# Performance work log

Measured on AMD Instinct MI355X. Metric: run time of the kernel, lower is better.

The kernel has to match this reference:

```python
import jax, jax.numpy as jnp
import numpy as np

B, S, D = 2, 2048, 4096
N_HEADS, N_KV_HEADS = 32, 8
HEAD_DIM = D // N_HEADS  # 128
N_REP = N_HEADS // N_KV_HEADS
NEG_INF = -1e9  # finite stand-in for -inf additive causal mask


def apply_rotary_emb(x, freqs_cis):
    # x: [b, s, h, hd]; freqs_cis: [s, hd//2, 2] (cos, sin)
    b, s, h, hd = x.shape
    xr = x.reshape(b, s, h, hd // 2, 2)
    fc = freqs_cis.reshape(1, s, 1, hd // 2, 2)
    o0 = xr[..., 0] * fc[..., 0] - xr[..., 1] * fc[..., 1]
    o1 = xr[..., 1] * fc[..., 0] + xr[..., 0] * fc[..., 1]
    return jnp.stack([o0, o1], axis=-1).reshape(b, s, h, hd)


def setup_inputs() -> dict:
    key = jax.random.key(0)
    ks = jax.random.split(key, 6)
    x = jax.random.normal(ks[0], (B, S, D), dtype=jnp.float32)
    # weights stored torch-style: [out_features, in_features]
    wq = jax.random.normal(ks[1], (N_HEADS * HEAD_DIM, D), dtype=jnp.float32) * 0.02
    wk = jax.random.normal(ks[2], (N_KV_HEADS * HEAD_DIM, D), dtype=jnp.float32) * 0.02
    wv = jax.random.normal(ks[3], (N_KV_HEADS * HEAD_DIM, D), dtype=jnp.float32) * 0.02
    wo = jax.random.normal(ks[4], (D, N_HEADS * HEAD_DIM), dtype=jnp.float32) * 0.02
    # rotary table (Llama-style, theta=10000)
    inv_freq = 1.0 / (10000.0 ** (np.arange(0, HEAD_DIM, 2, dtype=np.float32) / HEAD_DIM))
    angles = np.arange(S, dtype=np.float32)[:, None] * inv_freq[None, :]
    freqs_cis = jnp.asarray(np.stack([np.cos(angles), np.sin(angles)], axis=-1))  # [S, hd//2, 2]
    # additive causal mask
    mask = jnp.where(jnp.tril(jnp.ones((S, S), dtype=bool)), 0.0, NEG_INF).astype(jnp.float32)
    return {"x": x, "start_pos": 0, "freqs_cis": freqs_cis, "mask": mask,
            "wq": wq, "wk": wk, "wv": wv, "wo": wo}


def reference(x, start_pos, freqs_cis, mask, wq, wk, wv, wo):
    b, s, _ = x.shape
    xq = jnp.einsum('bsd,ed->bse', x, wq).reshape(b, s, N_HEADS, HEAD_DIM)
    xk = jnp.einsum('bsd,ed->bse', x, wk).reshape(b, s, N_KV_HEADS, HEAD_DIM)
    xv = jnp.einsum('bsd,ed->bse', x, wv).reshape(b, s, N_KV_HEADS, HEAD_DIM)
    xq = apply_rotary_emb(xq, freqs_cis)
    xk = apply_rotary_emb(xk, freqs_cis)
    # repeat_kv (repeat_interleave along head dim)
    xk = jnp.repeat(xk, N_REP, axis=2)
    xv = jnp.repeat(xv, N_REP, axis=2)
    q = xq.transpose(0, 2, 1, 3)  # [b, h, s, hd]
    k = xk.transpose(0, 2, 1, 3)
    v = xv.transpose(0, 2, 1, 3)
    scores = jnp.einsum('bhqd,bhkd->bhqk', q, k) / jnp.sqrt(jnp.float32(HEAD_DIM))
    scores = scores + mask[None, None, :, :]
    probs = jax.nn.softmax(scores.astype(jnp.float32), axis=-1).astype(q.dtype)
    out = jnp.einsum('bhqk,bhkd->bhqd', probs, v)
    out = out.transpose(0, 2, 1, 3).reshape(b, s, N_HEADS * HEAD_DIM)
    return jnp.einsum('bse,de->bsd', out, wo)
```

## Files before the change

kernel.cpp:

```cpp
#include <hip/hip_runtime.h>
#include <cstdint>
#include <cstddef>

#define B_   2
#define S_   2048
#define D_   4096
#define H_   32
#define KVH_ 8
#define HD_  128

typedef unsigned short u16;
typedef short     bf16x8 __attribute__((ext_vector_type(8)));
typedef float     f32x4  __attribute__((ext_vector_type(4)));
typedef float     f32x16 __attribute__((ext_vector_type(16)));
typedef u16       u16x8  __attribute__((ext_vector_type(8)));
typedef uint32_t  u32x2  __attribute__((ext_vector_type(2)));
typedef uint32_t  u32x4  __attribute__((ext_vector_type(4)));

__device__ __forceinline__ u16 f2bf(float f) {
  union { float f; uint32_t u; } v; v.f = f;
  uint32_t u = v.u;
  return (u16)((u + 0x7fffu + ((u >> 16) & 1u)) >> 16);
}
__device__ __forceinline__ float bf2f(u16 h) {
  union { uint32_t u; float f; } v; v.u = ((uint32_t)h) << 16;
  return v.f;
}
__device__ __forceinline__ uint32_t cvtpk(float lo, float hi_) {
  uint32_t r; asm("v_cvt_pk_bf16_f32 %0, %1, %2" : "=v"(r) : "v"(lo), "v"(hi_)); return r;
}
__device__ __forceinline__ float exp2v(float x) {
  float r; asm("v_exp_f32 %0, %1" : "=v"(r) : "v"(x)); return r;
}

__device__ __forceinline__ void gl_lds16(const void* g, void* l) {
  __builtin_amdgcn_global_load_lds(
      (const __attribute__((address_space(1))) void*)g,
      (__attribute__((address_space(3))) void*)l, 16, 0, 0);
}

#define MFMA(a, b, c)  __builtin_amdgcn_mfma_f32_16x16x32_bf16((a), (b), (c), 0, 0, 0)
#define MFMA32(a, b, c) __builtin_amdgcn_mfma_f32_32x32x16_bf16((a), (b), (c), 0, 0, 0)
#define PLSWAP(x, y) asm volatile("v_permlane32_swap_b32 %0, %1" : "+v"(x), "+v"(y))

__global__ void cast4_kernel(const float* __restrict__ x, const float* __restrict__ wq,
                             const float* __restrict__ wk, const float* __restrict__ wv,
                             u16* __restrict__ xb, u16* __restrict__ wqb,
                             u16* __restrict__ wkb, u16* __restrict__ wvb) {
  int i = blockIdx.x * 256 + threadIdx.x;
  const float* src; u16* dst; int off;
  if (i < 2097152)      { src = x;  dst = xb;  off = i; }
  else if (i < 4194304) { src = wq; dst = wqb; off = i - 2097152; }
  else if (i < 4718592) { src = wk; dst = wkb; off = i - 4194304; }
  else                  { src = wv; dst = wvb; off = i - 4718592; }
  const float4* p = (const float4*)src + (size_t)off * 2;
  float4 a = p[0], b = p[1];
  u16x8 r;
  r[0] = f2bf(a.x); r[1] = f2bf(a.y); r[2] = f2bf(a.z); r[3] = f2bf(a.w);
  r[4] = f2bf(b.x); r[5] = f2bf(b.y); r[6] = f2bf(b.z); r[7] = f2bf(b.w);
  *((u16x8*)dst + off) = r;
}

__global__ void cast_kernel(const float* __restrict__ in, u16* __restrict__ out, int n8) {
  int i = blockIdx.x * blockDim.x + threadIdx.x;
  if (i >= n8) return;
  const float4* p = (const float4*)in + (size_t)i * 2;
  float4 a = p[0], b = p[1];
  u16x8 r;
  r[0] = f2bf(a.x); r[1] = f2bf(a.y); r[2] = f2bf(a.z); r[3] = f2bf(a.w);
  r[4] = f2bf(b.x); r[5] = f2bf(b.y); r[6] = f2bf(b.z); r[7] = f2bf(b.w);
  *((u16x8*)out + i) = r;
}

template <bool OUT_F32>
__global__ __launch_bounds__(256, 2)
void gemm_bt(const u16* __restrict__ A, const u16* __restrict__ Bw,
             void* __restrict__ C, int M, int N, int K) {
  __shared__ u16 lA[128 * 32];
  __shared__ u16 lB[128 * 32];
  const int tid = threadIdx.x;
  const int w = tid >> 6, l = tid & 63;
  const int lc = l & 15, lg = l >> 4;
  const int bn = blockIdx.x, bm = blockIdx.y;
  const int wr = w >> 1, wc = w & 1;
  const u16* Ab = A + (size_t)(bm * 128) * K;
  const u16* Bb = Bw + (size_t)(bn * 128) * K;
  const int srow = l >> 2;
  const int scol = (l & 3) * 8;

  f32x4 acc[4][4];
#pragma unroll
  for (int i = 0; i < 4; ++i)
#pragma unroll
    for (int j = 0; j < 4; ++j) acc[i][j] = (f32x4){0.f, 0.f, 0.f, 0.f};

  const int nk = K >> 5;
  for (int kt = 0; kt < nk; ++kt) {
    const int k0 = kt * 32;
    __syncthreads();
#pragma unroll
    for (int i = 0; i < 2; ++i) {
      const int rowA = (w * 2 + i) * 16;
      gl_lds16(Ab + (size_t)(rowA + srow) * K + k0 + scol, &lA[rowA * 32]);
      gl_lds16(Bb + (size_t)(rowA + srow) * K + k0 + scol, &lB[rowA * 32]);
    }
    __syncthreads();
    bf16x8 af[4], bfr[4];
#pragma unroll
    for (int mi = 0; mi < 4; ++mi)
      af[mi] = *(const bf16x8*)&lA[(wr * 64 + mi * 16 + lc) * 32 + lg * 8];
#pragma unroll
    for (int ni = 0; ni < 4; ++ni)
      bfr[ni] = *(const bf16x8*)&lB[(wc * 64 + ni * 16 + lc) * 32 + lg * 8];
#pragma unroll
    for (int mi = 0; mi < 4; ++mi)
#pragma unroll
      for (int ni = 0; ni < 4; ++ni)
        acc[mi][ni] = MFMA(af[mi], bfr[ni], acc[mi][ni]);
  }

#pragma unroll
  for (int mi = 0; mi < 4; ++mi)
#pragma unroll
    for (int ni = 0; ni < 4; ++ni)
#pragma unroll
      for (int r = 0; r < 4; ++r) {
        const int row = bm * 128 + wr * 64 + mi * 16 + lg * 4 + r;
        const int col = bn * 128 + wc * 64 + ni * 16 + lc;
        if constexpr (OUT_F32)
          ((float*)C)[(size_t)row * N + col] = acc[mi][ni][r];
        else
          ((u16*)C)[(size_t)row * N + col] = f2bf(acc[mi][ni][r]);
      }
}

template <int MODE>
__global__ __launch_bounds__(512, 2)
void gemm256_bt(const u16* __restrict__ A, const u16* __restrict__ Bw,
                void* __restrict__ C, int M, int N, int K,
                const float* __restrict__ fr, float qscale) {
  __shared__ u16 sA[2 * 256 * 64];
  __shared__ u16 sB[2 * 256 * 64];
  const int tid = threadIdx.x;
  const int w = tid >> 6, l = tid & 63;
  const int lc = l & 15, lg = l >> 4;
  const int wm = w >> 2, wn = w & 3;
  const int nbn = N >> 8;
  const int nwg = (M >> 8) * nbn;
  const int cpx = nwg >> 3;
  const int lin = blockIdx.x;
  const int swz = (lin & 7) * cpx + (lin >> 3);
  const int bm = swz / nbn, bn = swz % nbn;
  const u16* Ab = A + (size_t)(bm * 256) * K;
  const u16* Bb = Bw + (size_t)(bn * 256) * K;
  const int lr = l >> 3;
  const int scc = ((l & 7) ^ lr) * 8;
  int cxg[2];
#pragma unroll
  for (int kk = 0; kk < 2; ++kk) cxg[kk] = ((kk * 4 + lg) ^ (lc & 7)) * 8;

  f32x4 acc[8][4];
#pragma unroll
  for (int i = 0; i < 8; ++i)
#pragma unroll
    for (int j = 0; j < 4; ++j) acc[i][j] = (f32x4){0.f, 0.f, 0.f, 0.f};

  auto STAGEA = [&](int buf, int t1, int h) {
    const int k0 = t1 * 64;
#pragma unroll
    for (int j = 0; j < 2; ++j) {
      const int r0 = h * 128 + w * 16 + j * 8;
      gl_lds16(Ab + (size_t)(r0 + lr) * K + k0 + scc, &sA[buf * 16384 + r0 * 64]);
    }
  };
  auto STAGEB = [&](int buf, int t1, int h) {
    const int k0 = t1 * 64;
#pragma unroll
    for (int j = 0; j < 2; ++j) {
      const int r0 = h * 128 + w * 16 + j * 8;
      gl_lds16(Bb + (size_t)(r0 + lr) * K + k0 + scc, &sB[buf * 16384 + r0 * 64]);
    }
  };

  bf16x8 a0r[4][2], a1r[4][2], b0r[2][2], b1r[2][2];
  auto LDA0 = [&](int cb) {
#pragma unroll
    for (int mi = 0; mi < 4; ++mi)
#pragma unroll
      for (int kk = 0; kk < 2; ++kk)
        a0r[mi][kk] = *(const bf16x8*)
            &sA[cb + (wm * 64 + mi * 16 + lc) * 64 + cxg[kk]];
  };
  auto LDA1 = [&](int cb) {
#pragma unroll
    for (int mi = 0; mi < 4; ++mi)
#pragma unroll
      for (int kk = 0; kk < 2; ++kk)
        a1r[mi][kk] = *(const bf16x8*)
            &sA[cb + (128 + wm * 64 + mi * 16 + lc) * 64 + cxg[kk]];
  };
  auto LDB0 = [&](int cb) {
#pragma unroll
    for (int ni = 0; ni < 2; ++ni)
#pragma unroll
      for (int kk = 0; kk < 2; ++kk)
        b0r[ni][kk] = *(const bf16x8*)
            &sB[cb + (wn * 32 + ni * 16 + lc) * 64 + cxg[kk]];
  };
  auto LDB1 = [&](int cb) {
#pragma unroll
    for (int ni = 0; ni < 2; ++ni)
#pragma unroll
      for (int kk = 0; kk < 2; ++kk)
        b1r[ni][kk] = *(const bf16x8*)
            &sB[cb + (128 + wn * 32 + ni * 16 + lc) * 64 + cxg[kk]];
  };

#define VMW(N_) asm volatile("s_waitcnt vmcnt(" #N_ ")" ::: "memory")
#define BARR do { __builtin_amdgcn_s_barrier(); asm volatile("" ::: "memory"); } while (0)
#define LGKM do { asm volatile("s_waitcnt lgkmcnt(0)" ::: "memory"); \
                  __builtin_amdgcn_sched_barrier(0); } while (0)
#define MMQ(AF, HA, HB, BF) do { __builtin_amdgcn_s_setprio(1); \
  _Pragma("unroll") for (int kk = 0; kk < 2; ++kk) \
  _Pragma("unroll") for (int mi = 0; mi < 4; ++mi) \
  _Pragma("unroll") for (int ni = 0; ni < 2; ++ni) \
    acc[(HA) * 4 + mi][(HB) * 2 + ni] = \
        MFMA(AF[mi][kk], BF[ni][kk], acc[(HA) * 4 + mi][(HB) * 2 + ni]); \
  __builtin_amdgcn_s_setprio(0); } while (0)

  const int nk = K >> 6;
  STAGEA(0, 0, 0); STAGEB(0, 0, 0);
  STAGEB(0, 0, 1); STAGEA(0, 0, 1);
  STAGEA(1, 1, 0); STAGEB(1, 1, 0);
  VMW(4);
  BARR;

  for (int t = 0; t < nk; ++t) {
    const int cur = t & 1;
    const int cb = cur * 16384;
    const int nb = cur ^ 1;
    const bool n1 = (t + 1 < nk), n2 = (t + 2 < nk);

    LDA0(cb); LDB0(cb);
    BARR;
    if (n1) { STAGEB(nb, t + 1, 1); STAGEA(nb, t + 1, 1); }
    LGKM;
    MMQ(a0r, 0, 0, b0r);

    LDB1(cb);
    BARR;
    LGKM;
    MMQ(a0r, 0, 1, b1r);

    LDA1(cb);
    BARR;
    if (n2) STAGEA(cur, t + 2, 0);
    LGKM;
    MMQ(a1r, 1, 1, b1r);

    if (n2) STAGEB(cur, t + 2, 0);
    MMQ(a1r, 1, 0, b0r);
    if (n1) {
      if (n2) VMW(4); else VMW(0);
      BARR;
    }
  }
#undef VMW
#undef BARR
#undef LGKM
#undef MMQ

#pragma unroll
  for (int ha = 0; ha < 2; ++ha)
#pragma unroll
    for (int mi = 0; mi < 4; ++mi)
#pragma unroll
      for (int hb = 0; hb < 2; ++hb)
#pragma unroll
        for (int ni = 0; ni < 2; ++ni)
#pragma unroll
          for (int r = 0; r < 4; ++r) {
            const int row = bm * 256 + ha * 128 + wm * 64 + mi * 16 + lg * 4 + r;
            const int col = bn * 256 + hb * 128 + wn * 32 + ni * 16 + lc;
            const float v = acc[ha * 4 + mi][hb * 2 + ni][r];
            if constexpr (MODE == 1) {
              ((float*)C)[(size_t)row * N + col] = v;
            } else if constexpr (MODE == 0) {
              ((u16*)C)[(size_t)row * N + col] = f2bf(v);
            } else {
              const float pv = __shfl_xor(v, 1, 64);
              const int b = row >> 11, s = row & (S_ - 1);
              const int h = col >> 7, d = col & 127;
              const float2 cs = ((const float2*)fr)[s * 64 + (d >> 1)];
              const float o = ((lc & 1) == 0) ? (v * cs.x - pv * cs.y)
                                              : (v * cs.x + pv * cs.y);
              ((u16*)C)[(((size_t)(b * H_ + h) * S_ + s)) * HD_ + d] =
                  f2bf(o * qscale);
            }
          }
}

template <int NH, int STRIDE, int OFF>
__global__ void rope_kernel(const u16* __restrict__ lin, const float* __restrict__ fr,
                            u16* __restrict__ out, float scale) {
  int idx = blockIdx.x * 256 + threadIdx.x;
  const int total = B_ * S_ * NH * 64;
  if (idx >= total) return;
  const int i = idx & 63;
  const int h = (idx >> 6) % NH;
  const int t = idx / (64 * NH);
  const int s = t & (S_ - 1);
  const int b = t >> 11;
  const size_t src = (size_t)t * STRIDE + OFF + h * HD_ + 2 * i;
  const float x0 = bf2f(lin[src]);
  const float x1 = bf2f(lin[src + 1]);
  const float2 cs = ((const float2*)fr)[s * 64 + i];
  const float o0 = (x0 * cs.x - x1 * cs.y) * scale;
  const float o1 = (x1 * cs.x + x0 * cs.y) * scale;
  const size_t dst = ((size_t)((b * NH + h) * S_ + s)) * HD_ + 2 * i;
  out[dst] = f2bf(o0);
  out[dst + 1] = f2bf(o1);
}

__global__ void vtrans_kernel(const u16* __restrict__ kvlin, u16* __restrict__ vt) {
  __shared__ u16 tile[32][33];
  const int tx = threadIdx.x, ty = threadIdx.y;
  const int s0 = blockIdx.x * 32;
  const int d0 = blockIdx.y * 32;
  const int bk = blockIdx.z;
  const int b = bk >> 3, kv = bk & 7;
#pragma unroll
  for (int r = 0; r < 4; ++r) {
    const int s = s0 + ty + r * 8;
    tile[ty + r * 8][tx] =
        kvlin[((size_t)(b * S_ + s)) * 2048 + 1024 + kv * HD_ + d0 + tx];
  }
  __syncthreads();
#pragma unroll
  for (int r = 0; r < 4; ++r) {
    const int d = d0 + ty + r * 8;
    vt[((size_t)bk * HD_ + d) * S_ + s0 + tx] = tile[tx][ty + r * 8];
  }
}

__global__ __launch_bounds__(256, 2)
void attn_kernel(const u16* __restrict__ Q, const u16* __restrict__ K,
                 const u16* __restrict__ V, u16* __restrict__ O) {
  __shared__ u16 sK[2][64 * HD_];
  __shared__ u16 sV[2][HD_ * 64];
  const int tid = threadIdx.x;
  const int w = tid >> 6, l = tid & 63;
  const int hi = l >> 5, q32 = l & 31;
  const int kv = blockIdx.y, b = blockIdx.z;
  const int h = kv * 4 + w;
  const u16* Kp = K + ((size_t)(b * KVH_ + kv) * S_) * HD_;
  const u16* Vp = V + ((size_t)(b * KVH_ + kv) * HD_) * S_;

  int koff[4], voff[4];
#pragma unroll
  for (int i = 0; i < 4; ++i) {
    const int kr = w * 16 + i * 4 + (l >> 4);
    koff[i] = kr * HD_ + (((l & 15) ^ (kr & 7))) * 8;
    const int vr = w * 32 + i * 8 + (l >> 3);
    voff[i] = vr * S_ + (((l & 7) ^ (vr & 7))) * 8;
  }
  int cx[8];
#pragma unroll
  for (int c = 0; c < 8; ++c) cx[c] = ((c * 2 + hi) ^ (l & 7)) * 8;

  auto STAGE = [&](int bufi, int ti) {
    const u16* kg = Kp + (size_t)ti * (64 * HD_);
    const u16* vg = Vp + (size_t)ti * 64;
#pragma unroll
    for (int i = 0; i < 4; ++i) {
      gl_lds16(kg + koff[i], &sK[bufi][(w * 16 + i * 4) * HD_]);
      gl_lds16(vg + voff[i], &sV[bufi][(w * 32 + i * 8) * 64]);
    }
  };

  int cur = 0;
  for (int seg = 0; seg < 2; ++seg) {
    const int qt = seg ? (63 - blockIdx.x) : blockIdx.x;
    const int qg = qt * 32 + q32;
    const u16* Qp = Q + ((size_t)(b * H_ + h) * S_ + qt * 32) * HD_;

    bf16x8 qf[8];
#pragma unroll
    for (int ds = 0; ds < 8; ++ds)
      qf[ds] = *(const bf16x8*)(Qp + (size_t)q32 * HD_ + ds * 16 + hi * 8);
    asm volatile("s_waitcnt vmcnt(0)" ::: "memory");

    f32x16 out[4];
#pragma unroll
    for (int d = 0; d < 4; ++d)
#pragma unroll
      for (int r = 0; r < 16; ++r) out[d][r] = 0.f;
    float mrun = -1e30f, lrun = 0.f;

    const int nt = (qt >> 1) + 1;
    STAGE(cur, 0);

    for (int t = 0; t < nt; ++t) {
      if (t + 1 < nt) {
        STAGE(cur ^ 1, t + 1);
        asm volatile("s_waitcnt vmcnt(8)" ::: "memory");
      } else {
        asm volatile("s_waitcnt vmcnt(0)" ::: "memory");
      }
      __builtin_amdgcn_s_barrier();
      asm volatile("" ::: "memory");

      f32x16 sc0, sc1;
#pragma unroll
      for (int r = 0; r < 16; ++r) { sc0[r] = 0.f; sc1[r] = 0.f; }
      __builtin_amdgcn_s_setprio(1);
#pragma unroll
      for (int ds = 0; ds < 8; ++ds) {
        bf16x8 kf0 = *(const bf16x8*)&sK[cur][q32 * HD_ + cx[ds]];
        bf16x8 kf1 = *(const bf16x8*)&sK[cur][(32 + q32) * HD_ + cx[ds]];
        sc0 = MFMA32(kf0, qf[ds], sc0);
        sc1 = MFMA32(kf1, qf[ds], sc1);
      }
      __builtin_amdgcn_s_setprio(0);

      const bool diag = (t == nt - 1);
      float p0[16], p1[16];
#pragma unroll
      for (int r = 0; r < 16; ++r) {
        const int krow = (r & 3) + 8 * (r >> 2) + 4 * hi;
        float v0 = sc0[r], v1 = sc1[r];
        if (diag) {
          if (t * 64 + krow > qg) v0 = -1e9f;
          if (t * 64 + 32 + krow > qg) v1 = -1e9f;
        }
        p0[r] = v0; p1[r] = v1;
      }
      float rm = -1e30f;
#pragma unroll
      for (int r = 0; r < 16; ++r) rm = fmaxf(rm, fmaxf(p0[r], p1[r]));
      rm = fmaxf(rm, __shfl_xor(rm, 32, 64));
      if (!__all(rm <= mrun + 8.0f)) {
        const float mnew = fmaxf(mrun, rm);
        const float alpha = exp2v(mrun - mnew);
        mrun = mnew;
        lrun *= alpha;
#pragma unroll
        for (int d = 0; d < 4; ++d) out[d] *= alpha;
      }
      float sum = 0.f;
#pragma unroll
      for (int r = 0; r < 16; ++r) {
        p0[r] = exp2v(p0[r] - mrun);
        p1[r] = exp2v(p1[r] - mrun);
        sum += p0[r] + p1[r];
      }
      sum += __shfl_xor(sum, 32, 64);
      lrun += sum;
      uint32_t pk0[8], pk1[8];
#pragma unroll
      for (int g = 0; g < 4; ++g) {
        pk0[2 * g]     = cvtpk(p0[4 * g], p0[4 * g + 1]);
        pk0[2 * g + 1] = cvtpk(p0[4 * g + 2], p0[4 * g + 3]);
        pk1[2 * g]     = cvtpk(p1[4 * g], p1[4 * g + 1]);
        pk1[2 * g + 1] = cvtpk(p1[4 * g + 2], p1[4 * g + 3]);
      }
      PLSWAP(pk0[0], pk0[2]); PLSWAP(pk0[1], pk0[3]);
      PLSWAP(pk0[4], pk0[6]); PLSWAP(pk0[5], pk0[7]);
      PLSWAP(pk1[0], pk1[2]); PLSWAP(pk1[1], pk1[3]);
      PLSWAP(pk1[4], pk1[6]); PLSWAP(pk1[5], pk1[7]);
      bf16x8 pa[4];
      pa[0] = __builtin_bit_cast(bf16x8, (u32x4){pk0[0], pk0[1], pk0[2], pk0[3]});
      pa[1] = __builtin_bit_cast(bf16x8, (u32x4){pk0[4], pk0[5], pk0[6], pk0[7]});
      pa[2] = __builtin_bit_cast(bf16x8, (u32x4){pk1[0], pk1[1], pk1[2], pk1[3]});
      pa[3] = __builtin_bit_cast(bf16x8, (u32x4){pk1[4], pk1[5], pk1[6], pk1[7]});
      __builtin_amdgcn_s_setprio(1);
#pragma unroll
      for (int d = 0; d < 4; ++d) {
        const int vbase = (d * 32 + q32) * 64;
#pragma unroll
        for (int kk = 0; kk < 4; ++kk) {
          bf16x8 vf = *(const bf16x8*)&sV[cur][vbase + cx[kk]];
          out[d] = MFMA32(vf, pa[kk], out[d]);
        }
      }
      __builtin_amdgcn_s_setprio(0);
      asm volatile("" ::: "memory");
      __builtin_amdgcn_s_barrier();
      cur ^= 1;
    }

    const float inv = 1.0f / lrun;
    u16* myS = ((u16*)sK) + w * 4096;
#pragma unroll
    for (int d = 0; d < 4; ++d)
#pragma unroll
      for (int rq = 0; rq < 4; ++rq) {
        u32x2 pw;
        pw[0] = cvtpk(out[d][rq * 4 + 0] * inv, out[d][rq * 4 + 1] * inv);
        pw[1] = cvtpk(out[d][rq * 4 + 2] * inv, out[d][rq * 4 + 3] * inv);
        const int gin = (d * 8 + rq * 2 + hi) ^ (q32 & 15);
        *(u32x2*)&myS[q32 * 128 + gin * 4] = pw;
      }
    asm volatile("s_waitcnt lgkmcnt(0)" ::: "memory");
    __builtin_amdgcn_sched_barrier(0);
    const int rr = l >> 4;
    const int cc = l & 15;
#pragma unroll
    for (int p = 0; p < 8; ++p) {
      const int q = p * 4 + rr;
      const int ga = (2 * cc) ^ (q & 15);
      const int gb = (2 * cc + 1) ^ (q & 15);
      u32x2 va = *(const u32x2*)&myS[q * 128 + ga * 4];
      u32x2 vb = *(const u32x2*)&myS[q * 128 + gb * 4];
      u32x4 val = {va[0], va[1], vb[0], vb[1]};
      *(u32x4*)&O[((size_t)(b * S_ + qt * 32 + q)) * (H_ * HD_) + h * HD_ + cc * 8] = val;
    }
    if (seg == 0) {
      asm volatile("" ::: "memory");
      __builtin_amdgcn_s_barrier();
    }
  }
}

extern "C" void kernel_launch(void* const* d_in, const int* in_sizes, int n_in,
                              void* d_out, int out_size, void* d_ws, size_t ws_size,
                              hipStream_t stream) {
  const float* x     = (const float*)d_in[0];
  const float* freqs = (const float*)d_in[2];
  const float* wq    = (const float*)d_in[4];
  const float* wk    = (const float*)d_in[5];
  const float* wv    = (const float*)d_in[6];
  const float* wo    = (const float*)d_in[7];

  char* ws = (char*)d_ws;
  u16* xb    = (u16*)(ws + 0);
  u16* wqb   = (u16*)(ws + 33554432);
  u16* wkb   = (u16*)(ws + 67108864);
  u16* wvb   = (u16*)(ws + 75497472);
  u16* qrope = (u16*)(ws + 83886080);
  u16* kvlin = (u16*)(ws + 117440512);
  u16* kr   = wkb;
  u16* vt   = wvb;
  u16* aout = wqb;
  u16* wob  = xb;

  const float qscale = 0.08838834764831845f * 1.4426950408889634f;

  cast4_kernel<<<20480, 256, 0, stream>>>(x, wq, wk, wv, xb, wqb, wkb, wvb);
  gemm256_bt<2><<<256, 512, 0, stream>>>(xb, wqb, qrope, 4096, 4096, 4096,
                                         freqs, qscale);
  gemm_bt<false><<<dim3(16, 32), 256, 0, stream>>>(xb, wkb, kvlin, 4096, 2048, 4096);
  rope_kernel<8, 2048, 0><<<8192, 256, 0, stream>>>(kvlin, freqs, kr, 1.0f);
  vtrans_kernel<<<dim3(64, 4, 16), dim3(32, 8), 0, stream>>>(kvlin, vt);
  attn_kernel<<<dim3(32, 8, 2), 256, 0, stream>>>(qrope, kr, vt, aout);
  cast_kernel<<<8192, 256, 0, stream>>>(wo, wob, 2097152);
  gemm256_bt<1><<<256, 512, 0, stream>>>(aout, wob, d_out, 4096, 4096, 4096,
                                         nullptr, 0.f);
}
```

Measured before the change: 514.1 us.

## Fuse K rotary embedding into KV GEMM epilogue and move main-loop barrier

The separate rope_kernel for K is removed. The K/V projection GEMM now applies the rotary embedding in its epilogue and writes K directly in head-major layout, while V goes to a separate linear buffer that is then transposed. This drops one launch and one read/write pass over K. Separately, the 256-tile GEMM's vmcnt wait and barrier move from the end of each iteration to the start, and the barriers are repositioned before the LDS reads. That changes how LDS reads and global prefetch overlap, and the barrier reordering carries some risk of an LDS hazard.

```diff
diff --git a/kernel.cpp b/kernel.cpp
--- a/kernel.cpp
+++ b/kernel.cpp
@@ -72,10 +72,10 @@
   *((u16x8*)out + i) = r;
 }
 
-template <bool OUT_F32>
 __global__ __launch_bounds__(256, 2)
-void gemm_bt(const u16* __restrict__ A, const u16* __restrict__ Bw,
-             void* __restrict__ C, int M, int N, int K) {
+void gemm_kv(const u16* __restrict__ A, const u16* __restrict__ Bw,
+             u16* __restrict__ Kout, u16* __restrict__ Vout,
+             int M, int N, int K, const float* __restrict__ fr) {
   __shared__ u16 lA[128 * 32];
   __shared__ u16 lB[128 * 32];
   const int tid = threadIdx.x;
@@ -127,10 +127,18 @@
       for (int r = 0; r < 4; ++r) {
         const int row = bm * 128 + wr * 64 + mi * 16 + lg * 4 + r;
         const int col = bn * 128 + wc * 64 + ni * 16 + lc;
-        if constexpr (OUT_F32)
-          ((float*)C)[(size_t)row * N + col] = acc[mi][ni][r];
-        else
-          ((u16*)C)[(size_t)row * N + col] = f2bf(acc[mi][ni][r]);
+        const float v = acc[mi][ni][r];
+        if (col < 1024) {
+          const float pv = __shfl_xor(v, 1, 64);
+          const int s = row & (S_ - 1), b = row >> 11;
+          const int kv = col >> 7, d = col & 127;
+          const float2 cs = ((const float2*)fr)[s * 64 + (d >> 1)];
+          const float o = ((lc & 1) == 0) ? (v * cs.x - pv * cs.y)
+                                          : (v * cs.x + pv * cs.y);
+          Kout[((size_t)(b * KVH_ + kv) * S_ + s) * HD_ + d] = f2bf(o);
+        } else {
+          Vout[(size_t)row * 1024 + (col - 1024)] = f2bf(v);
+        }
       }
 }
 
@@ -232,8 +240,6 @@
   STAGEA(0, 0, 0); STAGEB(0, 0, 0);
   STAGEB(0, 0, 1); STAGEA(0, 0, 1);
   STAGEA(1, 1, 0); STAGEB(1, 1, 0);
-  VMW(4);
-  BARR;
 
   for (int t = 0; t < nk; ++t) {
     const int cur = t & 1;
@@ -241,29 +247,26 @@
     const int nb = cur ^ 1;
     const bool n1 = (t + 1 < nk), n2 = (t + 2 < nk);
 
+    if (n1) VMW(4); else VMW(0);
+    BARR;
     LDA0(cb); LDB0(cb);
-    BARR;
     if (n1) { STAGEB(nb, t + 1, 1); STAGEA(nb, t + 1, 1); }
     LGKM;
     MMQ(a0r, 0, 0, b0r);
 
+    BARR;
     LDB1(cb);
-    BARR;
     LGKM;
     MMQ(a0r, 0, 1, b1r);
 
+    BARR;
     LDA1(cb);
-    BARR;
     if (n2) STAGEA(cur, t + 2, 0);
     LGKM;
     MMQ(a1r, 1, 1, b1r);
 
     if (n2) STAGEB(cur, t + 2, 0);
     MMQ(a1r, 1, 0, b0r);
-    if (n1) {
-      if (n2) VMW(4); else VMW(0);
-      BARR;
-    }
   }
 #undef VMW
 #undef BARR
@@ -300,29 +303,7 @@
           }
 }
 
-template <int NH, int STRIDE, int OFF>
-__global__ void rope_kernel(const u16* __restrict__ lin, const float* __restrict__ fr,
-                            u16* __restrict__ out, float scale) {
-  int idx = blockIdx.x * 256 + threadIdx.x;
-  const int total = B_ * S_ * NH * 64;
-  if (idx >= total) return;
-  const int i = idx & 63;
-  const int h = (idx >> 6) % NH;
-  const int t = idx / (64 * NH);
-  const int s = t & (S_ - 1);
-  const int b = t >> 11;
-  const size_t src = (size_t)t * STRIDE + OFF + h * HD_ + 2 * i;
-  const float x0 = bf2f(lin[src]);
-  const float x1 = bf2f(lin[src + 1]);
-  const float2 cs = ((const float2*)fr)[s * 64 + i];
-  const float o0 = (x0 * cs.x - x1 * cs.y) * scale;
-  const float o1 = (x1 * cs.x + x0 * cs.y) * scale;
-  const size_t dst = ((size_t)((b * NH + h) * S_ + s)) * HD_ + 2 * i;
-  out[dst] = f2bf(o0);
-  out[dst + 1] = f2bf(o1);
-}
-
-__global__ void vtrans_kernel(const u16* __restrict__ kvlin, u16* __restrict__ vt) {
+__global__ void vtrans_kernel(const u16* __restrict__ vlin, u16* __restrict__ vt) {
   __shared__ u16 tile[32][33];
   const int tx = threadIdx.x, ty = threadIdx.y;
   const int s0 = blockIdx.x * 32;
@@ -333,7 +314,7 @@
   for (int r = 0; r < 4; ++r) {
     const int s = s0 + ty + r * 8;
     tile[ty + r * 8][tx] =
-        kvlin[((size_t)(b * S_ + s)) * 2048 + 1024 + kv * HD_ + d0 + tx];
+        vlin[((size_t)(b * S_ + s)) * 1024 + kv * HD_ + d0 + tx];
   }
   __syncthreads();
 #pragma unroll
@@ -538,8 +519,8 @@
   u16* wkb   = (u16*)(ws + 67108864);
   u16* wvb   = (u16*)(ws + 75497472);
   u16* qrope = (u16*)(ws + 83886080);
-  u16* kvlin = (u16*)(ws + 117440512);
-  u16* kr   = wkb;
+  u16* kr    = (u16*)(ws + 117440512);
+  u16* vlin  = (u16*)(ws + 125829120);
   u16* vt   = wvb;
   u16* aout = wqb;
   u16* wob  = xb;
@@ -549,9 +530,9 @@
   cast4_kernel<<<20480, 256, 0, stream>>>(x, wq, wk, wv, xb, wqb, wkb, wvb);
   gemm256_bt<2><<<256, 512, 0, stream>>>(xb, wqb, qrope, 4096, 4096, 4096,
                                          freqs, qscale);
-  gemm_bt<false><<<dim3(16, 32), 256, 0, stream>>>(xb, wkb, kvlin, 4096, 2048, 4096);
-  rope_kernel<8, 2048, 0><<<8192, 256, 0, stream>>>(kvlin, freqs, kr, 1.0f);
-  vtrans_kernel<<<dim3(64, 4, 16), dim3(32, 8), 0, stream>>>(kvlin, vt);
+  gemm_kv<<<dim3(16, 32), 256, 0, stream>>>(xb, wkb, kr, vlin, 4096, 2048, 4096,
+                                            freqs);
+  vtrans_kernel<<<dim3(64, 4, 16), dim3(32, 8), 0, stream>>>(vlin, vt);
   attn_kernel<<<dim3(32, 8, 2), 256, 0, stream>>>(qrope, kr, vt, aout);
   cast_kernel<<<8192, 256, 0, stream>>>(wo, wob, 2097152);
   gemm256_bt<1><<<256, 512, 0, stream>>>(aout, wob, d_out, 4096, 4096, 4096,
```

After: 497.1 us. 3.3% less time.

## Switch 256-tile GEMM to 32x32x16 MFMA and move barriers before LDS reads

Applied to the files above, without the earlier changes.

Rewrites the 256x256 GEMM inner loop to use 32x32 MFMA instructions with f32x16 accumulators instead of 16x16 ones. This changes the LDS fragment loads, the swizzle index and the epilogue row/column mapping to match. The larger MFMA shape issues fewer instructions and does more work per LDS read. The wait-for-data barrier is also moved from the end of each iteration to the start, and the other barriers now precede each fragment load. This reorders the synchronisation and risks hazards on LDS buffer reuse.

```diff
diff --git a/kernel.cpp b/kernel.cpp
--- a/kernel.cpp
+++ b/kernel.cpp
@@ -143,7 +143,7 @@
   __shared__ u16 sB[2 * 256 * 64];
   const int tid = threadIdx.x;
   const int w = tid >> 6, l = tid & 63;
-  const int lc = l & 15, lg = l >> 4;
+  const int q32l = l & 31, hi32 = l >> 5;
   const int wm = w >> 2, wn = w & 3;
   const int nbn = N >> 8;
   const int nwg = (M >> 8) * nbn;
@@ -155,15 +155,19 @@
   const u16* Bb = Bw + (size_t)(bn * 256) * K;
   const int lr = l >> 3;
   const int scc = ((l & 7) ^ lr) * 8;
-  int cxg[2];
-#pragma unroll
-  for (int kk = 0; kk < 2; ++kk) cxg[kk] = ((kk * 4 + lg) ^ (lc & 7)) * 8;
-
-  f32x4 acc[8][4];
-#pragma unroll
-  for (int i = 0; i < 8; ++i)
-#pragma unroll
-    for (int j = 0; j < 4; ++j) acc[i][j] = (f32x4){0.f, 0.f, 0.f, 0.f};
+  int cx32[4];
+#pragma unroll
+  for (int s = 0; s < 4; ++s) cx32[s] = ((s * 2 + hi32) ^ (l & 7)) * 8;
+
+  f32x16 acc[2][2][2];
+#pragma unroll
+  for (int i = 0; i < 2; ++i)
+#pragma unroll
+    for (int j = 0; j < 2; ++j)
+#pragma unroll
+      for (int k2 = 0; k2 < 2; ++k2)
+#pragma unroll
+        for (int r = 0; r < 16; ++r) acc[i][j][k2][r] = 0.f;
 
   auto STAGEA = [&](int buf, int t1, int h) {
     const int k0 = t1 * 64;
@@ -182,38 +186,34 @@
     }
   };
 
-  bf16x8 a0r[4][2], a1r[4][2], b0r[2][2], b1r[2][2];
+  bf16x8 a0r[2][4], a1r[2][4], b0r[4], b1r[4];
   auto LDA0 = [&](int cb) {
 #pragma unroll
-    for (int mi = 0; mi < 4; ++mi)
-#pragma unroll
-      for (int kk = 0; kk < 2; ++kk)
-        a0r[mi][kk] = *(const bf16x8*)
-            &sA[cb + (wm * 64 + mi * 16 + lc) * 64 + cxg[kk]];
+    for (int rt = 0; rt < 2; ++rt)
+#pragma unroll
+      for (int s = 0; s < 4; ++s)
+        a0r[rt][s] = *(const bf16x8*)
+            &sA[cb + (wm * 64 + rt * 32 + q32l) * 64 + cx32[s]];
   };
   auto LDA1 = [&](int cb) {
 #pragma unroll
-    for (int mi = 0; mi < 4; ++mi)
-#pragma unroll
-      for (int kk = 0; kk < 2; ++kk)
-        a1r[mi][kk] = *(const bf16x8*)
-            &sA[cb + (128 + wm * 64 + mi * 16 + lc) * 64 + cxg[kk]];
+    for (int rt = 0; rt < 2; ++rt)
+#pragma unroll
+      for (int s = 0; s < 4; ++s)
+        a1r[rt][s] = *(const bf16x8*)
+            &sA[cb + (128 + wm * 64 + rt * 32 + q32l) * 64 + cx32[s]];
   };
   auto LDB0 = [&](int cb) {
 #pragma unroll
-    for (int ni = 0; ni < 2; ++ni)
-#pragma unroll
-      for (int kk = 0; kk < 2; ++kk)
-        b0r[ni][kk] = *(const bf16x8*)
-            &sB[cb + (wn * 32 + ni * 16 + lc) * 64 + cxg[kk]];
+    for (int s = 0; s < 4; ++s)
+      b0r[s] = *(const bf16x8*)
+          &sB[cb + (wn * 32 + q32l) * 64 + cx32[s]];
   };
   auto LDB1 = [&](int cb) {
 #pragma unroll
-    for (int ni = 0; ni < 2; ++ni)
-#pragma unroll
-      for (int kk = 0; kk < 2; ++kk)
-        b1r[ni][kk] = *(const bf16x8*)
-            &sB[cb + (128 + wn * 32 + ni * 16 + lc) * 64 + cxg[kk]];
+    for (int s = 0; s < 4; ++s)
+      b1r[s] = *(const bf16x8*)
+          &sB[cb + (128 + wn * 32 + q32l) * 64 + cx32[s]];
   };
 
 #define VMW(N_) asm volatile("s_waitcnt vmcnt(" #N_ ")" ::: "memory")
@@ -221,19 +221,15 @@
 #define LGKM do { asm volatile("s_waitcnt lgkmcnt(0)" ::: "memory"); \
                   __builtin_amdgcn_sched_barrier(0); } while (0)
 #define MMQ(AF, HA, HB, BF) do { __builtin_amdgcn_s_setprio(1); \
-  _Pragma("unroll") for (int kk = 0; kk < 2; ++kk) \
-  _Pragma("unroll") for (int mi = 0; mi < 4; ++mi) \
-  _Pragma("unroll") for (int ni = 0; ni < 2; ++ni) \
-    acc[(HA) * 4 + mi][(HB) * 2 + ni] = \
-        MFMA(AF[mi][kk], BF[ni][kk], acc[(HA) * 4 + mi][(HB) * 2 + ni]); \
+  _Pragma("unroll") for (int s = 0; s < 4; ++s) \
+  _Pragma("unroll") for (int rt = 0; rt < 2; ++rt) \
+    acc[HA][HB][rt] = MFMA32(AF[rt][s], BF[s], acc[HA][HB][rt]); \
   __builtin_amdgcn_s_setprio(0); } while (0)
 
   const int nk = K >> 6;
   STAGEA(0, 0, 0); STAGEB(0, 0, 0);
   STAGEB(0, 0, 1); STAGEA(0, 0, 1);
   STAGEA(1, 1, 0); STAGEB(1, 1, 0);
-  VMW(4);
-  BARR;
 
   for (int t = 0; t < nk; ++t) {
     const int cur = t & 1;
@@ -241,29 +237,26 @@
     const int nb = cur ^ 1;
     const bool n1 = (t + 1 < nk), n2 = (t + 2 < nk);
 
+    if (n1) VMW(4); else VMW(0);
+    BARR;
     LDA0(cb); LDB0(cb);
-    BARR;
     if (n1) { STAGEB(nb, t + 1, 1); STAGEA(nb, t + 1, 1); }
     LGKM;
     MMQ(a0r, 0, 0, b0r);
 
+    BARR;
     LDB1(cb);
-    BARR;
     LGKM;
     MMQ(a0r, 0, 1, b1r);
 
+    BARR;
     LDA1(cb);
-    BARR;
     if (n2) STAGEA(cur, t + 2, 0);
     LGKM;
     MMQ(a1r, 1, 1, b1r);
 
     if (n2) STAGEB(cur, t + 2, 0);
     MMQ(a1r, 1, 0, b0r);
-    if (n1) {
-      if (n2) VMW(4); else VMW(0);
-      BARR;
-    }
   }
 #undef VMW
 #undef BARR
@@ -273,31 +266,30 @@
 #pragma unroll
   for (int ha = 0; ha < 2; ++ha)
 #pragma unroll
-    for (int mi = 0; mi < 4; ++mi)
-#pragma unroll
-      for (int hb = 0; hb < 2; ++hb)
-#pragma unroll
-        for (int ni = 0; ni < 2; ++ni)
-#pragma unroll
-          for (int r = 0; r < 4; ++r) {
-            const int row = bm * 256 + ha * 128 + wm * 64 + mi * 16 + lg * 4 + r;
-            const int col = bn * 256 + hb * 128 + wn * 32 + ni * 16 + lc;
-            const float v = acc[ha * 4 + mi][hb * 2 + ni][r];
-            if constexpr (MODE == 1) {
-              ((float*)C)[(size_t)row * N + col] = v;
-            } else if constexpr (MODE == 0) {
-              ((u16*)C)[(size_t)row * N + col] = f2bf(v);
-            } else {
-              const float pv = __shfl_xor(v, 1, 64);
-              const int b = row >> 11, s = row & (S_ - 1);
-              const int h = col >> 7, d = col & 127;
-              const float2 cs = ((const float2*)fr)[s * 64 + (d >> 1)];
-              const float o = ((lc & 1) == 0) ? (v * cs.x - pv * cs.y)
-                                              : (v * cs.x + pv * cs.y);
-              ((u16*)C)[(((size_t)(b * H_ + h) * S_ + s)) * HD_ + d] =
-                  f2bf(o * qscale);
-            }
+    for (int hb = 0; hb < 2; ++hb)
+#pragma unroll
+      for (int rt = 0; rt < 2; ++rt)
+#pragma unroll
+        for (int r = 0; r < 16; ++r) {
+          const int row = bm * 256 + ha * 128 + wm * 64 + rt * 32 +
+                          (r & 3) + 8 * (r >> 2) + 4 * hi32;
+          const int col = bn * 256 + hb * 128 + wn * 32 + q32l;
+          const float v = acc[ha][hb][rt][r];
+          if constexpr (MODE == 1) {
+            ((float*)C)[(size_t)row * N + col] = v;
+          } else if constexpr (MODE == 0) {
+            ((u16*)C)[(size_t)row * N + col] = f2bf(v);
+          } else {
+            const float pv = __shfl_xor(v, 1, 64);
+            const int b = row >> 11, s = row & (S_ - 1);
+            const int h = col >> 7, d = col & 127;
+            const float2 cs = ((const float2*)fr)[s * 64 + (d >> 1)];
+            const float o = ((l & 1) == 0) ? (v * cs.x - pv * cs.y)
+                                           : (v * cs.x + pv * cs.y);
+            ((u16*)C)[(((size_t)(b * H_ + h) * S_ + s)) * HD_ + d] =
+                f2bf(o * qscale);
           }
+        }
 }
 
 template <int NH, int STRIDE, int OFF>
```

Result: no change. 518.8 us (+0.9%).
